# Performance work log

Hardware: AMD Instinct MI355X
Metric: run time of the kernel (lower is better)

## Reference

```python
import jax, jax.numpy as jnp
import numpy as np

KERNEL = 3
PAD = 1
STRIDE = 1

def setup_inputs() -> dict:
    key = jax.random.key(0)
    k1, k2 = jax.random.split(key)
    x = jax.random.normal(k1, (32, 128, 56, 56), dtype=jnp.float32)
    # xavier_uniform-like init for weight
    fan_in = 128 * KERNEL * KERNEL
    fan_out = 256 * KERNEL * KERNEL
    limit = float(np.sqrt(6.0 / (fan_in + fan_out)))
    weight = jax.random.uniform(k2, (256, 128, KERNEL, KERNEL), dtype=jnp.float32,
                                minval=-limit, maxval=limit)
    bias = jnp.zeros((256,), dtype=jnp.float32)
    return {"x": x, "weight": weight, "bias": bias}

def reference(x, weight, bias):
    # Equivalent to the per-pixel im2col matmul loop: a standard 3x3 conv,
    # stride 1, symmetric padding 1, plus per-channel bias.
    out = jax.lax.conv_general_dilated(
        x, weight,
        window_strides=(STRIDE, STRIDE),
        padding=((PAD, PAD), (PAD, PAD)),
        dimension_numbers=("NCHW", "OIHW", "NCHW"),
    )
    return out + bias[None, :, None, None]
```

## Files before the change

### kernel.cpp

```cpp
#include <hip/hip_runtime.h>
#include <hip/hip_bf16.h>
#include <stdint.h>
#include <stddef.h>

#define NIMG 32
#define C_IN 128
#define C_OUT 256
#define HW 56
#define SP 3136
#define STOT (NIMG * SP)
#define PD 58
#define KTOT 1152

#define BM 256
#define BN 224
#define NSLICE 36
#define THREADS 512

typedef __attribute__((ext_vector_type(8))) short bf16x8;
typedef __attribute__((ext_vector_type(4))) float f32x4;

__device__ __forceinline__ void gload16(const void* g, void* l) {
    __builtin_amdgcn_global_load_lds(
        (const __attribute__((address_space(1))) void*)g,
        (__attribute__((address_space(3))) void*)l,
        16, 0, 0);
}

#define BAR() do { asm volatile("" ::: "memory"); \
                   __builtin_amdgcn_s_barrier();  \
                   asm volatile("" ::: "memory"); } while (0)
#define VMCNT(n) asm volatile("s_waitcnt vmcnt(" #n ")" ::: "memory")

__device__ __forceinline__ unsigned short bf2u(float f) {
    __hip_bfloat16 b = __float2bfloat16(f);
    return *reinterpret_cast<unsigned short*>(&b);
}

#define PAD_BLOCKS (NIMG * PD)
#define WT_BLOCKS  ((9 * C_OUT * C_IN) / 256)

__global__ __launch_bounds__(256)
void prep_kernel(const float* __restrict__ x, const float* __restrict__ wgt,
                 __hip_bfloat16* __restrict__ xp, __hip_bfloat16* __restrict__ wt) {
    __shared__ float t[C_IN][HW + 1];
    const int b = blockIdx.x;
    if (b < PAD_BLOCKS) {
        const int hp = b % PD;
        const int n  = b / PD;
        const int h  = hp - 1;
        const bool interior = ((unsigned)h < (unsigned)HW);
        if (interior) {
            for (int idx = threadIdx.x; idx < C_IN * HW; idx += 256) {
                int ci = idx / HW, w = idx - ci * HW;
                t[ci][w] = x[((size_t)n * C_IN + ci) * SP + h * HW + w];
            }
        }
        __syncthreads();
        ushort4* dst = (ushort4*)(xp + ((size_t)n * PD + hp) * PD * C_IN);
        for (int idx = threadIdx.x; idx < PD * C_IN / 4; idx += 256) {
            int el = idx * 4;
            int wp = el >> 7, c0 = el & 127;
            ushort4 v = {0, 0, 0, 0};
            if (interior && wp >= 1 && wp <= HW) {
                int w = wp - 1;
                v.x = bf2u(t[c0 + 0][w]);
                v.y = bf2u(t[c0 + 1][w]);
                v.z = bf2u(t[c0 + 2][w]);
                v.w = bf2u(t[c0 + 3][w]);
            }
            dst[idx] = v;
        }
    } else {
        int idx = (b - PAD_BLOCKS) * 256 + threadIdx.x;
        int ci  = idx & 127;
        int co  = (idx >> 7) & 255;
        int tap = idx >> 15;
        wt[idx] = __float2bfloat16(wgt[(co * C_IN + ci) * 9 + tap]);
    }
}

__global__ __launch_bounds__(THREADS, 2)
void conv_mfma_kernel(const __hip_bfloat16* __restrict__ xp,
                      const __hip_bfloat16* __restrict__ wt,
                      const float* __restrict__ bias,
                      float* __restrict__ out) {
    extern __shared__ short smem[];

    const int tid  = threadIdx.x;
    const int lane = tid & 63;
    const int wid  = tid >> 6;
    const int rl   = lane & 15;
    const int kq   = lane >> 4;
    const int wg   = (blockIdx.x & 7) * 56 + (blockIdx.x >> 3);
    const int s0   = wg * BN;

    const int cg_el = (((lane & 3) ^ ((lane >> 3) & 3)) << 3);
    const int srow  = wid * 16 + (lane >> 2);
    const int aS0   = srow * C_IN + cg_el;
    const int aS1   = aS0 + 128 * C_IN;
    const int ldsw  = wid * 512;
    int s_r = s0 + srow;
    int n_  = s_r / SP, rem = s_r - n_ * SP;
    int h_  = rem / HW, w_ = rem - h_ * HW;
    const int bS0 = ((n_ * PD + h_) * PD + w_) * C_IN + cg_el;
    int srow2 = 128 + srow; if (srow2 > BN - 1) srow2 = BN - 1;
    s_r = s0 + srow2;
    n_ = s_r / SP; rem = s_r - n_ * SP; h_ = rem / HW; w_ = rem - h_ * HW;
    const int bS1 = ((n_ * PD + h_) * PD + w_) * C_IN + cg_el;

    const int rch = ((kq ^ ((lane >> 1) & 3)) << 3);
    const int wm  = (wid >> 1) * 64;
    const int wn  = (wid & 1) * 112;
    const int aRd = (wm + rl) * 32 + rch;
    const int bRd = (wn + rl) * 32 + rch;

    auto STG = [&](int s) {
        int tap = s >> 2, ci0 = (s & 3) << 5;
        const __hip_bfloat16* wsrc = wt + tap * (C_OUT * C_IN) + ci0;
        short* Ad = smem + (s & 3) * 16384 + ldsw;
        gload16(wsrc + aS0, Ad);
        gload16(wsrc + aS1, Ad + 4096);
        int kh = (tap * 11) >> 5, kw = tap - kh * 3;
        const __hip_bfloat16* xsrc = xp + (kh * PD + kw) * C_IN + ci0;
        short* Bd = smem + (s & 3) * 16384 + 8192 + ldsw;
        gload16(xsrc + bS0, Bd);
        gload16(xsrc + bS1, Bd + 4096);
    };
    auto RD = [&](bf16x8* fa, bf16x8* fb, int r) {
        const short* Ab = smem + r * 16384;
        const short* Bb = Ab + 8192;
        #pragma unroll
        for (int j = 0; j < 4; ++j) fa[j] = *(const bf16x8*)(Ab + aRd + j * 512);
        #pragma unroll
        for (int j = 0; j < 7; ++j) fb[j] = *(const bf16x8*)(Bb + bRd + j * 512);
    };

    float bv[4][4];
    #pragma unroll
    for (int mi = 0; mi < 4; ++mi)
        #pragma unroll
        for (int j = 0; j < 4; ++j)
            bv[mi][j] = bias[wm + mi * 16 + (kq << 2) + j];

    f32x4 acc[4][7] = {};
    bf16x8 fa0[4], fb0[7], fa1[4], fb1[7];

    #define MM(FA, FB) do { \
        __builtin_amdgcn_s_setprio(1); \
        _Pragma("unroll") \
        for (int mi = 0; mi < 4; ++mi) \
            _Pragma("unroll") \
            for (int ni = 0; ni < 7; ++ni) \
                acc[mi][ni] = __builtin_amdgcn_mfma_f32_16x16x32_bf16( \
                    FA[mi], FB[ni], acc[mi][ni], 0, 0, 0); \
        __builtin_amdgcn_s_setprio(0); \
    } while (0)

    STG(0); STG(1); STG(2);
    VMCNT(8);
    BAR();
    RD(fa0, fb0, 0);

    for (int t = 0; t < 18; ++t) {
        if (t == 17) { VMCNT(0); } else { VMCNT(4); }
        BAR();
        RD(fa1, fb1, (2 * t + 1) & 3);
        if (t <= 16) STG(2 * t + 3);
        MM(fa0, fb0);

        if (t < 17) {
            VMCNT(4);
            BAR();
            RD(fa0, fb0, (2 * t + 2) & 3);
            if (t <= 15) STG(2 * t + 4);
            MM(fa1, fb1);
        } else {
            BAR();
            MM(fa1, fb1);
        }
    }
    #undef MM

    #pragma unroll
    for (int ni = 0; ni < 7; ++ni) {
        int s  = s0 + wn + ni * 16 + rl;
        int n  = s / SP;
        int si = s - n * SP;
        float* obase = out + (size_t)n * C_OUT * SP + si;
        #pragma unroll
        for (int mi = 0; mi < 4; ++mi) {
            int cob = wm + mi * 16 + (kq << 2);
            #pragma unroll
            for (int j = 0; j < 4; ++j) {
                obase[(size_t)(cob + j) * SP] = acc[mi][ni][j] + bv[mi][j];
            }
        }
    }
}

__global__ void conv_direct_kernel(const float* __restrict__ x,
                                   const float* __restrict__ wgt,
                                   const float* __restrict__ bias,
                                   float* __restrict__ out) {
    long idx = (long)blockIdx.x * 256 + threadIdx.x;
    if (idx >= (long)NIMG * C_OUT * SP) return;
    int si = (int)(idx % SP);
    int co = (int)((idx / SP) % C_OUT);
    int n  = (int)(idx / ((long)SP * C_OUT));
    int h = si / HW, w = si - (si / HW) * HW;
    float acc = bias[co];
    for (int ci = 0; ci < C_IN; ++ci) {
        const float* xr = x + ((size_t)n * C_IN + ci) * SP;
        const float* wr = wgt + ((size_t)co * C_IN + ci) * 9;
        #pragma unroll
        for (int kh = 0; kh < 3; ++kh) {
            int ih = h + kh - 1;
            if (ih < 0 || ih >= HW) continue;
            #pragma unroll
            for (int kw = 0; kw < 3; ++kw) {
                int iw = w + kw - 1;
                if (iw < 0 || iw >= HW) continue;
                acc += xr[ih * HW + iw] * wr[kh * 3 + kw];
            }
        }
    }
    out[idx] = acc;
}

extern "C" void kernel_launch(void* const* d_in, const int* in_sizes, int n_in,
                              void* d_out, int out_size, void* d_ws, size_t ws_size,
                              hipStream_t stream) {
    const float* x    = (const float*)d_in[0];
    const float* wgt  = (const float*)d_in[1];
    const float* bias = (const float*)d_in[2];
    float* out = (float*)d_out;

    const size_t xp_bytes = (size_t)NIMG * PD * PD * C_IN * sizeof(__hip_bfloat16);
    const size_t wt_bytes = (size_t)9 * C_OUT * C_IN * sizeof(__hip_bfloat16);

    if (ws_size >= xp_bytes + wt_bytes) {
        __hip_bfloat16* xp  = (__hip_bfloat16*)d_ws;
        __hip_bfloat16* wtb = (__hip_bfloat16*)((char*)d_ws + xp_bytes);

        prep_kernel<<<PAD_BLOCKS + WT_BLOCKS, 256, 0, stream>>>(x, wgt, xp, wtb);

        hipFuncSetAttribute((const void*)conv_mfma_kernel,
                            hipFuncAttributeMaxDynamicSharedMemorySize, 131072);
        conv_mfma_kernel<<<STOT / BN, THREADS, 131072, stream>>>(xp, wtb, bias, out);
    } else {
        long total = (long)NIMG * C_OUT * SP;
        conv_direct_kernel<<<(int)((total + 255) / 256), 256, 0, stream>>>(
            x, wgt, bias, out);
    }
}
```

Before: 84.99 us.

## Load weight fragments directly from global in MFMA-ready layout, bypassing LDS

The prep kernel now writes weights pre-arranged per K-slice and 16-row fragment, laid out exactly as each lane's MFMA A-operand. The conv kernel loads these fragments straight from global/L2 into registers instead of staging them through LDS, which halves the LDS footprint per block from 128KB to 64KB. The goal is to cut LDS traffic and store/read work for the A operand and to allow more residency. In exchange, the main loop now waits on global-load latency for A fragments, and the vmcnt accounting is changed to cover these extra loads.

```diff
diff --git a/kernel.cpp b/kernel.cpp
--- a/kernel.cpp
+++ b/kernel.cpp
@@ -38,11 +38,11 @@
 }
 
 #define PAD_BLOCKS (NIMG * PD)
-#define WT_BLOCKS  ((9 * C_OUT * C_IN) / 256)
+#define A_BLOCKS   (NSLICE * 16 * 64 / 256)
 
 __global__ __launch_bounds__(256)
 void prep_kernel(const float* __restrict__ x, const float* __restrict__ wgt,
-                 __hip_bfloat16* __restrict__ xp, __hip_bfloat16* __restrict__ wt) {
+                 __hip_bfloat16* __restrict__ xp, __hip_bfloat16* __restrict__ aarr) {
     __shared__ float t[C_IN][HW + 1];
     const int b = blockIdx.x;
     if (b < PAD_BLOCKS) {
@@ -73,16 +73,30 @@
         }
     } else {
         int idx = (b - PAD_BLOCKS) * 256 + threadIdx.x;
-        int ci  = idx & 127;
-        int co  = (idx >> 7) & 255;
-        int tap = idx >> 15;
-        wt[idx] = __float2bfloat16(wgt[(co * C_IN + ci) * 9 + tap]);
+        int l   = idx & 63;
+        int f   = (idx >> 6) & 15;
+        int s   = idx >> 10;
+        int tap = s >> 2;
+        int co  = f * 16 + (l & 15);
+        int cib = ((s & 3) << 5) + ((l >> 4) << 3);
+        ushort4 v0, v1;
+        v0.x = bf2u(wgt[(co * C_IN + cib + 0) * 9 + tap]);
+        v0.y = bf2u(wgt[(co * C_IN + cib + 1) * 9 + tap]);
+        v0.z = bf2u(wgt[(co * C_IN + cib + 2) * 9 + tap]);
+        v0.w = bf2u(wgt[(co * C_IN + cib + 3) * 9 + tap]);
+        v1.x = bf2u(wgt[(co * C_IN + cib + 4) * 9 + tap]);
+        v1.y = bf2u(wgt[(co * C_IN + cib + 5) * 9 + tap]);
+        v1.z = bf2u(wgt[(co * C_IN + cib + 6) * 9 + tap]);
+        v1.w = bf2u(wgt[(co * C_IN + cib + 7) * 9 + tap]);
+        ushort4* d = (ushort4*)(aarr + (size_t)idx * 8);
+        d[0] = v0;
+        d[1] = v1;
     }
 }
 
 __global__ __launch_bounds__(THREADS, 2)
 void conv_mfma_kernel(const __hip_bfloat16* __restrict__ xp,
-                      const __hip_bfloat16* __restrict__ wt,
+                      const short* __restrict__ Aarr,
                       const float* __restrict__ bias,
                       float* __restrict__ out) {
     extern __shared__ short smem[];
@@ -97,8 +111,6 @@
 
     const int cg_el = (((lane & 3) ^ ((lane >> 3) & 3)) << 3);
     const int srow  = wid * 16 + (lane >> 2);
-    const int aS0   = srow * C_IN + cg_el;
-    const int aS1   = aS0 + 128 * C_IN;
     const int ldsw  = wid * 512;
     int s_r = s0 + srow;
     int n_  = s_r / SP, rem = s_r - n_ * SP;
@@ -112,28 +124,28 @@
     const int rch = ((kq ^ ((lane >> 1) & 3)) << 3);
     const int wm  = (wid >> 1) * 64;
     const int wn  = (wid & 1) * 112;
-    const int aRd = (wm + rl) * 32 + rch;
     const int bRd = (wn + rl) * 32 + rch;
+    const int fbase = (wid >> 1) * 4;
 
     auto STG = [&](int s) {
         int tap = s >> 2, ci0 = (s & 3) << 5;
-        const __hip_bfloat16* wsrc = wt + tap * (C_OUT * C_IN) + ci0;
-        short* Ad = smem + (s & 3) * 16384 + ldsw;
-        gload16(wsrc + aS0, Ad);
-        gload16(wsrc + aS1, Ad + 4096);
         int kh = (tap * 11) >> 5, kw = tap - kh * 3;
         const __hip_bfloat16* xsrc = xp + (kh * PD + kw) * C_IN + ci0;
-        short* Bd = smem + (s & 3) * 16384 + 8192 + ldsw;
+        short* Bd = smem + (s & 3) * 8192 + ldsw;
         gload16(xsrc + bS0, Bd);
         gload16(xsrc + bS1, Bd + 4096);
     };
-    auto RD = [&](bf16x8* fa, bf16x8* fb, int r) {
-        const short* Ab = smem + r * 16384;
-        const short* Bb = Ab + 8192;
-        #pragma unroll
-        for (int j = 0; j < 4; ++j) fa[j] = *(const bf16x8*)(Ab + aRd + j * 512);
-        #pragma unroll
-        for (int j = 0; j < 7; ++j) fb[j] = *(const bf16x8*)(Bb + bRd + j * 512);
+    auto LDA = [&](bf16x8* ga, int s) {
+        const short* base = Aarr + ((size_t)((s * 16 + fbase) * 64 + lane)) * 8;
+        #pragma unroll
+        for (int mi = 0; mi < 4; ++mi)
+            ga[mi] = *(const bf16x8*)(base + mi * 512);
+    };
+    auto RD = [&](bf16x8* fb, int r) {
+        const short* Bb = smem + r * 8192;
+        #pragma unroll
+        for (int j = 0; j < 7; ++j)
+            fb[j] = *(const bf16x8*)(Bb + bRd + j * 512);
     };
 
     float bv[4][4];
@@ -144,40 +156,43 @@
             bv[mi][j] = bias[wm + mi * 16 + (kq << 2) + j];
 
     f32x4 acc[4][7] = {};
-    bf16x8 fa0[4], fb0[7], fa1[4], fb1[7];
-
-    #define MM(FA, FB) do { \
+    bf16x8 ga0[4], ga1[4], fb0[7], fb1[7];
+
+    #define MM(GA, FB) do { \
         __builtin_amdgcn_s_setprio(1); \
         _Pragma("unroll") \
         for (int mi = 0; mi < 4; ++mi) \
             _Pragma("unroll") \
             for (int ni = 0; ni < 7; ++ni) \
                 acc[mi][ni] = __builtin_amdgcn_mfma_f32_16x16x32_bf16( \
-                    FA[mi], FB[ni], acc[mi][ni], 0, 0, 0); \
+                    GA[mi], FB[ni], acc[mi][ni], 0, 0, 0); \
         __builtin_amdgcn_s_setprio(0); \
     } while (0)
 
     STG(0); STG(1); STG(2);
+    LDA(ga0, 0);
     VMCNT(8);
     BAR();
-    RD(fa0, fb0, 0);
+    RD(fb0, 0);
 
     for (int t = 0; t < 18; ++t) {
-        if (t == 17) { VMCNT(0); } else { VMCNT(4); }
+        const int p0 = 2 * t;
+        if (t == 17) { VMCNT(4); } else { VMCNT(6); }
         BAR();
-        RD(fa1, fb1, (2 * t + 1) & 3);
-        if (t <= 16) STG(2 * t + 3);
-        MM(fa0, fb0);
+        RD(fb1, (p0 + 1) & 3);
+        LDA(ga1, p0 + 1);
+        if (p0 <= 32) STG(p0 + 3);
+        MM(ga0, fb0);
 
         if (t < 17) {
-            VMCNT(4);
+            VMCNT(6);
             BAR();
-            RD(fa0, fb0, (2 * t + 2) & 3);
-            if (t <= 15) STG(2 * t + 4);
-            MM(fa1, fb1);
+            RD(fb0, (p0 + 2) & 3);
+            LDA(ga0, p0 + 2);
+            if (p0 + 1 <= 32) STG(p0 + 4);
+            MM(ga1, fb1);
         } else {
-            BAR();
-            MM(fa1, fb1);
+            MM(ga1, fb1);
         }
     }
     #undef MM
@@ -237,17 +252,18 @@
     float* out = (float*)d_out;
 
     const size_t xp_bytes = (size_t)NIMG * PD * PD * C_IN * sizeof(__hip_bfloat16);
-    const size_t wt_bytes = (size_t)9 * C_OUT * C_IN * sizeof(__hip_bfloat16);
-
-    if (ws_size >= xp_bytes + wt_bytes) {
-        __hip_bfloat16* xp  = (__hip_bfloat16*)d_ws;
-        __hip_bfloat16* wtb = (__hip_bfloat16*)((char*)d_ws + xp_bytes);
-
-        prep_kernel<<<PAD_BLOCKS + WT_BLOCKS, 256, 0, stream>>>(x, wgt, xp, wtb);
+    const size_t aa_bytes = (size_t)NSLICE * 16 * 64 * 8 * sizeof(__hip_bfloat16);
+
+    if (ws_size >= xp_bytes + aa_bytes) {
+        __hip_bfloat16* xp = (__hip_bfloat16*)d_ws;
+        __hip_bfloat16* aa = (__hip_bfloat16*)((char*)d_ws + xp_bytes);
+
+        prep_kernel<<<PAD_BLOCKS + A_BLOCKS, 256, 0, stream>>>(x, wgt, xp, aa);
 
         hipFuncSetAttribute((const void*)conv_mfma_kernel,
-                            hipFuncAttributeMaxDynamicSharedMemorySize, 131072);
-        conv_mfma_kernel<<<STOT / BN, THREADS, 131072, stream>>>(xp, wtb, bias, out);
+                            hipFuncAttributeMaxDynamicSharedMemorySize, 65536);
+        conv_mfma_kernel<<<STOT / BN, THREADS, 65536, stream>>>(
+            xp, (const short*)aa, bias, out);
     } else {
         long total = (long)NIMG * C_OUT * SP;
         conv_direct_kernel<<<(int)((total + 255) / 256), 256, 0, stream>>>(
```

After: 95.43 us. 12.3% more time.

## Load padded input window once into LDS and reuse across all nine taps

Applied to the files above, without the earlier changes.

The implicit-GEMM conv now loads a 6-row padded input window (4 output rows plus halo) for one image into LDS once, with an XOR swizzle, and reads the B fragments for all nine taps from that resident window. The old code re-streamed B slices from global memory for every tap. The output-channel tile is halved to 128, giving 896 blocks, and only weight slices are streamed through an 8-deep ring buffer. This removes repeated global/L2 traffic for the input, at the cost of the input being loaded twice (once per M half) and fewer MFMAs per fragment read.

```diff
diff --git a/kernel.cpp b/kernel.cpp
--- a/kernel.cpp
+++ b/kernel.cpp
@@ -12,10 +12,13 @@
 #define PD 58
 #define KTOT 1152
 
-#define BM 256
+#define BM 128
 #define BN 224
-#define NSLICE 36
+#define NTILE 896
 #define THREADS 512
+#define WIN_SH 44544
+#define ABUF_SH 4096
+#define LDS_BYTES (2 * (WIN_SH + 8 * ABUF_SH))
 
 typedef __attribute__((ext_vector_type(8))) short bf16x8;
 typedef __attribute__((ext_vector_type(4))) float f32x4;
@@ -31,6 +34,7 @@
                    __builtin_amdgcn_s_barrier();  \
                    asm volatile("" ::: "memory"); } while (0)
 #define VMCNT(n) asm volatile("s_waitcnt vmcnt(" #n ")" ::: "memory")
+#define LGKM0() asm volatile("s_waitcnt lgkmcnt(0)" ::: "memory")
 
 __device__ __forceinline__ unsigned short bf2u(float f) {
     __hip_bfloat16 b = __float2bfloat16(f);
@@ -86,111 +90,118 @@
                       const float* __restrict__ bias,
                       float* __restrict__ out) {
     extern __shared__ short smem[];
+    short* smemA = smem + WIN_SH;
 
     const int tid  = threadIdx.x;
     const int lane = tid & 63;
     const int wid  = tid >> 6;
     const int rl   = lane & 15;
     const int kq   = lane >> 4;
-    const int wg   = (blockIdx.x & 7) * 56 + (blockIdx.x >> 3);
-    const int s0   = wg * BN;
+
+    const int gt  = (blockIdx.x & 7) * 112 + (blockIdx.x >> 3);
+    const int m0  = gt & 1;
+    const int nt  = gt >> 1;
+    const int img = nt / 14;
+    const int R0  = (nt - img * 14) * 4;
+    const int s0  = nt * BN;
 
     const int cg_el = (((lane & 3) ^ ((lane >> 3) & 3)) << 3);
     const int srow  = wid * 16 + (lane >> 2);
-    const int aS0   = srow * C_IN + cg_el;
-    const int aS1   = aS0 + 128 * C_IN;
-    const int ldsw  = wid * 512;
-    int s_r = s0 + srow;
-    int n_  = s_r / SP, rem = s_r - n_ * SP;
-    int h_  = rem / HW, w_ = rem - h_ * HW;
-    const int bS0 = ((n_ * PD + h_) * PD + w_) * C_IN + cg_el;
-    int srow2 = 128 + srow; if (srow2 > BN - 1) srow2 = BN - 1;
-    s_r = s0 + srow2;
-    n_ = s_r / SP; rem = s_r - n_ * SP; h_ = rem / HW; w_ = rem - h_ * HW;
-    const int bS1 = ((n_ * PD + h_) * PD + w_) * C_IN + cg_el;
-
     const int rch = ((kq ^ ((lane >> 1) & 3)) << 3);
-    const int wm  = (wid >> 1) * 64;
+    const int wmA = (wid >> 1) * 32;
     const int wn  = (wid & 1) * 112;
-    const int aRd = (wm + rl) * 32 + rch;
-    const int bRd = (wn + rl) * 32 + rch;
-
-    auto STG = [&](int s) {
-        int tap = s >> 2, ci0 = (s & 3) << 5;
-        const __hip_bfloat16* wsrc = wt + tap * (C_OUT * C_IN) + ci0;
-        short* Ad = smem + (s & 3) * 16384 + ldsw;
-        gload16(wsrc + aS0, Ad);
-        gload16(wsrc + aS1, Ad + 4096);
-        int kh = (tap * 11) >> 5, kw = tap - kh * 3;
-        const __hip_bfloat16* xsrc = xp + (kh * PD + kw) * C_IN + ci0;
-        short* Bd = smem + (s & 3) * 16384 + 8192 + ldsw;
-        gload16(xsrc + bS0, Bd);
-        gload16(xsrc + bS1, Bd + 4096);
+    const int aRd = (wmA + rl) * 32 + rch;
+
+    int wrb[7], wc0[7];
+    #pragma unroll
+    for (int ni = 0; ni < 7; ++ni) {
+        int soff = wn + ni * 16 + rl;
+        int lr   = soff / 56;
+        int wc   = soff - lr * 56;
+        wrb[ni]  = lr * 58 + wc;
+        wc0[ni]  = wc;
+    }
+
+    auto STG_A = [&](int s) {
+        const __hip_bfloat16* src = wt + ((s >> 2) << 15)
+            + (((m0 << 7) + srow) << 7) + ((s & 3) << 5) + cg_el;
+        gload16(src, smemA + (s & 7) * ABUF_SH + wid * 512);
     };
-    auto RD = [&](bf16x8* fa, bf16x8* fb, int r) {
-        const short* Ab = smem + r * 16384;
-        const short* Bb = Ab + 8192;
-        #pragma unroll
-        for (int j = 0; j < 4; ++j) fa[j] = *(const bf16x8*)(Ab + aRd + j * 512);
-        #pragma unroll
-        for (int j = 0; j < 7; ++j) fb[j] = *(const bf16x8*)(Bb + bRd + j * 512);
-    };
-
-    float bv[4][4];
+
+    {
+        const int xbase = ((img * PD) + R0) * PD * C_IN;
+        for (int g = wid; g < 87; g += 8) {
+            int e    = g * 512 + (lane << 3);
+            int r    = e / 7424;
+            int rem  = e - r * 7424;
+            int wcol = rem >> 7;
+            int c    = (rem >> 3) & 15;
+            int csw  = c ^ (wcol & 7);
+            gload16(xp + xbase + e + ((csw - c) << 3), smem + g * 512);
+        }
+        #pragma unroll
+        for (int s = 0; s < 6; ++s) STG_A(s);
+    }
+
+    float bv[2][4];
     #pragma unroll
-    for (int mi = 0; mi < 4; ++mi)
+    for (int mi = 0; mi < 2; ++mi)
         #pragma unroll
         for (int j = 0; j < 4; ++j)
-            bv[mi][j] = bias[wm + mi * 16 + (kq << 2) + j];
-
-    f32x4 acc[4][7] = {};
-    bf16x8 fa0[4], fb0[7], fa1[4], fb1[7];
-
-    #define MM(FA, FB) do { \
-        __builtin_amdgcn_s_setprio(1); \
-        _Pragma("unroll") \
-        for (int mi = 0; mi < 4; ++mi) \
-            _Pragma("unroll") \
-            for (int ni = 0; ni < 7; ++ni) \
-                acc[mi][ni] = __builtin_amdgcn_mfma_f32_16x16x32_bf16( \
-                    FA[mi], FB[ni], acc[mi][ni], 0, 0, 0); \
-        __builtin_amdgcn_s_setprio(0); \
-    } while (0)
-
-    STG(0); STG(1); STG(2);
-    VMCNT(8);
-    BAR();
-    RD(fa0, fb0, 0);
-
-    for (int t = 0; t < 18; ++t) {
-        if (t == 17) { VMCNT(0); } else { VMCNT(4); }
+            bv[mi][j] = bias[(m0 << 7) + wmA + mi * 16 + (kq << 2) + j];
+
+    f32x4 acc[2][7] = {};
+
+    for (int h = 0; h < 18; ++h) {
+        if (h < 16)       { VMCNT(4); }
+        else if (h == 16) { VMCNT(2); }
+        else              { VMCNT(0); }
+        LGKM0();
         BAR();
-        RD(fa1, fb1, (2 * t + 1) & 3);
-        if (t <= 16) STG(2 * t + 3);
-        MM(fa0, fb0);
-
-        if (t < 17) {
-            VMCNT(4);
-            BAR();
-            RD(fa0, fb0, (2 * t + 2) & 3);
-            if (t <= 15) STG(2 * t + 4);
-            MM(fa1, fb1);
-        } else {
-            BAR();
-            MM(fa1, fb1);
-        }
-    }
-    #undef MM
+        if (h <= 14) { STG_A(2 * h + 6); STG_A(2 * h + 7); }
+
+        const int tap    = h >> 1;
+        const int kh     = (tap * 11) >> 5;
+        const int kw     = tap - kh * 3;
+        const int tapoff = kh * 58 + kw;
+        const int kbase  = (h & 1) << 1;
+
+        bf16x8 fa[2][2], fb[2][7];
+        #pragma unroll
+        for (int u = 0; u < 2; ++u) {
+            const int s = (tap << 2) + kbase + u;
+            const short* Ab = smemA + (s & 7) * ABUF_SH;
+            #pragma unroll
+            for (int mi = 0; mi < 2; ++mi)
+                fa[u][mi] = *(const bf16x8*)(Ab + aRd + mi * 512);
+            const int cqb = ((kbase + u) << 2) + kq;
+            #pragma unroll
+            for (int ni = 0; ni < 7; ++ni) {
+                int eb = (wrb[ni] + tapoff) << 7;
+                int sw = (wc0[ni] + kw) & 7;
+                fb[u][ni] = *(const bf16x8*)(smem + eb + ((cqb ^ sw) << 3));
+            }
+        }
+        __builtin_amdgcn_s_setprio(1);
+        #pragma unroll
+        for (int u = 0; u < 2; ++u)
+            #pragma unroll
+            for (int mi = 0; mi < 2; ++mi)
+                #pragma unroll
+                for (int ni = 0; ni < 7; ++ni)
+                    acc[mi][ni] = __builtin_amdgcn_mfma_f32_16x16x32_bf16(
+                        fa[u][mi], fb[u][ni], acc[mi][ni], 0, 0, 0);
+        __builtin_amdgcn_s_setprio(0);
+    }
 
     #pragma unroll
     for (int ni = 0; ni < 7; ++ni) {
         int s  = s0 + wn + ni * 16 + rl;
-        int n  = s / SP;
-        int si = s - n * SP;
-        float* obase = out + (size_t)n * C_OUT * SP + si;
-        #pragma unroll
-        for (int mi = 0; mi < 4; ++mi) {
-            int cob = wm + mi * 16 + (kq << 2);
+        int si = s - img * SP;
+        float* obase = out + (size_t)img * C_OUT * SP + si;
+        #pragma unroll
+        for (int mi = 0; mi < 2; ++mi) {
+            int cob = (m0 << 7) + wmA + mi * 16 + (kq << 2);
             #pragma unroll
             for (int j = 0; j < 4; ++j) {
                 obase[(size_t)(cob + j) * SP] = acc[mi][ni][j] + bv[mi][j];
@@ -246,8 +257,8 @@
         prep_kernel<<<PAD_BLOCKS + WT_BLOCKS, 256, 0, stream>>>(x, wgt, xp, wtb);
 
         hipFuncSetAttribute((const void*)conv_mfma_kernel,
-                            hipFuncAttributeMaxDynamicSharedMemorySize, 131072);
-        conv_mfma_kernel<<<STOT / BN, THREADS, 131072, stream>>>(xp, wtb, bias, out);
+                            hipFuncAttributeMaxDynamicSharedMemorySize, LDS_BYTES);
+        conv_mfma_kernel<<<NTILE, THREADS, LDS_BYTES, stream>>>(xp, wtb, bias, out);
     } else {
         long total = (long)NIMG * C_OUT * SP;
         conv_direct_kernel<<<(int)((total + 255) / 256), 256, 0, stream>>>(
```

After: 104.5 us. 23.0% more time.
